# Optimization experiments

Measured on AMD Instinct MI355X. Metric: run time of the kernel, lower is better.

Reference implementation:

```python
import jax, jax.numpy as jnp
import numpy as np

D_MODEL = 1024
NUM_HEADS = 16
D_HEAD = D_MODEL // NUM_HEADS


def setup_inputs() -> dict:
    key = jax.random.key(0)
    ks = jax.random.split(key, 5)
    b, n = 4, 2048
    x = jax.random.normal(ks[0], (b, n, D_MODEL), dtype=jnp.float32)
    s = 1.0 / np.sqrt(D_MODEL)
    w_qkv = jax.random.normal(ks[1], (D_MODEL, 3 * D_MODEL), dtype=jnp.float32) * s
    b_qkv = jax.random.normal(ks[2], (3 * D_MODEL,), dtype=jnp.float32) * 0.01
    w_out = jax.random.normal(ks[3], (D_MODEL, D_MODEL), dtype=jnp.float32) * s
    b_out = jax.random.normal(ks[4], (D_MODEL,), dtype=jnp.float32) * 0.01
    return {"x": x, "w_qkv": w_qkv, "b_qkv": b_qkv, "w_out": w_out, "b_out": b_out}


def reference(x, w_qkv, b_qkv, w_out, b_out):
    b, n, _ = x.shape
    h, d = NUM_HEADS, D_HEAD
    scale = d ** -0.5
    qkv = x @ w_qkv + b_qkv                       # [b, n, 3*d_model]
    # split as (qkv, h, d) on the feature axis, matching 'b n (qkv h d)'
    qkv = qkv.reshape(b, n, 3, h, d).transpose(2, 0, 3, 1, 4)  # [3, b, h, n, d]
    q, k, v = qkv[0], qkv[1], qkv[2]
    dots = jnp.einsum('bhid,bhjd->bhij', q, k) * scale
    causal = jnp.tril(jnp.ones((n, n), dtype=bool))
    dots = jnp.where(causal[None, None], dots, -jnp.inf)
    attn = jax.nn.softmax(dots, axis=-1)
    out = jnp.einsum('bhij,bhjd->bhid', attn, v)
    out = out.transpose(0, 2, 1, 3).reshape(b, n, h * d)
    return out @ w_out + b_out
```

## Files before the change

kernel.cpp:

```cpp
#include <hip/hip_runtime.h>
#include <hip/hip_bf16.h>
#include <stdint.h>

typedef unsigned short u16;
typedef __attribute__((ext_vector_type(8))) short bf16x8;
typedef __attribute__((ext_vector_type(4))) float f32x4;
typedef __attribute__((ext_vector_type(16))) float f32x16;
typedef __attribute__((ext_vector_type(4))) short s16x4;
typedef __attribute__((ext_vector_type(2))) unsigned u32x2;

#define SEQ   2048
#define BATCH 4

#define MFMA16(a,b,c) __builtin_amdgcn_mfma_f32_16x16x32_bf16(a,b,c,0,0,0)
#define MFMA32(a,b,c) __builtin_amdgcn_mfma_f32_32x32x16_bf16(a,b,c,0,0,0)
#define EXP2F __builtin_amdgcn_exp2f

__device__ __forceinline__ u16 f2bf(float f) {
  union { float f; uint32_t u; } c{f};
  uint32_t r = c.u + 0x7fffu + ((c.u >> 16) & 1u);
  return (u16)(r >> 16);
}

__device__ __forceinline__ void gll16(const void* g, void* l) {
  __builtin_amdgcn_global_load_lds((const __attribute__((address_space(1))) void*)g,
                                   (__attribute__((address_space(3))) void*)l,
                                   16, 0, 0);
}

__device__ __forceinline__ void plswap(uint32_t &a, uint32_t &b) {
  u32x2 r = __builtin_amdgcn_permlane32_swap(a, b, false, false);
  a = r[0]; b = r[1];
}
__device__ __forceinline__ float xhalf_max(float v) {
  union { float f; uint32_t u; } c{v};
  u32x2 r = __builtin_amdgcn_permlane32_swap(c.u, c.u, false, false);
  union { uint32_t u; float f; } x{r[0]}, y{r[1]};
  return fmaxf(x.f, y.f);
}
__device__ __forceinline__ float xhalf_add(float v) {
  union { float f; uint32_t u; } c{v};
  u32x2 r = __builtin_amdgcn_permlane32_swap(c.u, c.u, false, false);
  union { uint32_t u; float f; } x{r[0]}, y{r[1]};
  return x.f + y.f;
}

__global__ __launch_bounds__(256) void k_prep(const float* __restrict__ x,
                                              u16* __restrict__ xbf,
                                              const float* __restrict__ wqkv,
                                              u16* __restrict__ wqkvT,
                                              const float* __restrict__ wout,
                                              u16* __restrict__ woutT) {
  __shared__ float tl[32][33];
  const int bid = blockIdx.x, t = threadIdx.x;
  if (bid < 4096) {
    int i = (bid * 256 + t) * 8;
    float4 a = *(const float4*)(x + i);
    float4 b = *(const float4*)(x + i + 4);
    union { u16 u[8]; bf16x8 v; } r;
    r.u[0] = f2bf(a.x); r.u[1] = f2bf(a.y); r.u[2] = f2bf(a.z); r.u[3] = f2bf(a.w);
    r.u[4] = f2bf(b.x); r.u[5] = f2bf(b.y); r.u[6] = f2bf(b.z); r.u[7] = f2bf(b.w);
    *(bf16x8*)(xbf + i) = r.v;
    return;
  }
  const float* in; u16* out; int N, idx, nx;
  if (bid < 4096 + 3072) { in = wqkv; out = wqkvT; N = 3072; idx = bid - 4096; nx = 96; }
  else                   { in = wout; out = woutT; N = 1024; idx = bid - 7168; nx = 32; }
  const int K = 1024;
  const int c0 = (idx % nx) * 32, r0 = (idx / nx) * 32;
  const int tx = t & 31, ty = t >> 5;
#pragma unroll
  for (int j = 0; j < 32; j += 8)
    tl[ty + j][tx] = in[(size_t)(r0 + ty + j) * N + c0 + tx];
  __syncthreads();
#pragma unroll
  for (int j = 0; j < 32; j += 8)
    out[(size_t)(c0 + ty + j) * K + r0 + tx] = f2bf(tl[tx][ty + j]);
}

#define SBAR  asm volatile("s_barrier" ::: "memory")
#define LGKM0 asm volatile("s_waitcnt lgkmcnt(0)" ::: "memory")
#define VM2   asm volatile("s_waitcnt vmcnt(2)" ::: "memory")
#define VM0   asm volatile("s_waitcnt vmcnt(0)" ::: "memory")
#define FEN   asm volatile("" ::: "memory")

template<int OUT_F32, int VSPLIT>
__global__ __launch_bounds__(512, 2) void k_gemm256(const u16* __restrict__ A,
                                                    const u16* __restrict__ BT,
                                                    const float* __restrict__ bias,
                                                    void* __restrict__ Cv,
                                                    u16* __restrict__ vT,
                                                    int N, int K, int NT, int TN) {
  __shared__ alignas(16) char LDS[98304];
  const int t = threadIdx.x;
  const int l = t & 63, w = t >> 6;
  const int wm = w >> 2, wn = w & 3;
  const int lr = l & 15, lg = l >> 4;

  const int nwg = gridDim.x;
  const int cpx = nwg >> 3;
  const int sb = (blockIdx.x & 7) * cpx + (blockIdx.x >> 3);
  const int brow = (sb / TN) * 256, bcol = (sb % TN) * 128;

  auto stageA = [&](int c, int h, int tt) {
#pragma unroll
    for (int i = 0; i < 2; i++) {
      int s = t + i * 512;
      int r = s >> 3, cg = s & 7;
      int grow = brow + (r >> 6) * 128 + h * 64 + (r & 63);
      int gk = tt * 64 + ((cg ^ (r & 7)) * 8);
      gll16(A + (size_t)grow * K + gk, LDS + c * 49152 + h * 16384 + s * 16);
    }
  };
  auto stageB = [&](int c, int tt) {
#pragma unroll
    for (int i = 0; i < 2; i++) {
      int s = t + i * 512;
      int r = s >> 3, cg = s & 7;
      int grow = bcol + r;
      int gk = tt * 64 + ((cg ^ (r & 7)) * 8);
      gll16(BT + (size_t)grow * K + gk, LDS + c * 49152 + 32768 + s * 16);
    }
  };

  f32x4 acc[8][2] = {};
  bf16x8 afr[4], bfr[2];

#define READ_A(c, h, ks)                                                       \
  {                                                                            \
    const char* baseA = LDS + (c) * 49152 + (h) * 16384 + (wm * 64) * 128;     \
    _Pragma("unroll") for (int mi = 0; mi < 4; mi++)                           \
      afr[mi] = *(const bf16x8*)(baseA + (mi * 16 + lr) * 128 +                \
                                 ((((ks) * 4 + lg) ^ (lr & 7)) * 16));         \
  }
#define READ_B(c, ks)                                                          \
  {                                                                            \
    const char* baseB = LDS + (c) * 49152 + 32768 + (wn * 32) * 128;           \
    _Pragma("unroll") for (int ni = 0; ni < 2; ni++)                           \
      bfr[ni] = *(const bf16x8*)(baseB + (ni * 16 + lr) * 128 +                \
                                 ((((ks) * 4 + lg) ^ (lr & 7)) * 16));         \
  }
#define DO_MFMA(H)                                                             \
  {                                                                            \
    __builtin_amdgcn_s_setprio(1);                                             \
    _Pragma("unroll") for (int mi = 0; mi < 4; mi++)                           \
      _Pragma("unroll") for (int ni = 0; ni < 2; ni++)                         \
        acc[(H)*4 + mi][ni] = MFMA16(afr[mi], bfr[ni], acc[(H)*4 + mi][ni]);   \
    __builtin_amdgcn_s_setprio(0);                                             \
  }

  stageA(0, 0, 0); FEN;
  stageB(0, 0);    FEN;
  stageA(0, 1, 0); FEN;
  VM2; SBAR;

  for (int tt = 0; tt < NT; tt++) {
    const int c = tt & 1;
    if (tt + 1 < NT) { stageA(c ^ 1, 0, tt + 1); FEN; }
    READ_A(c, 0, 0); READ_B(c, 0);
    DO_MFMA(0);
    if (tt + 1 < NT) { VM2; } else { VM0; }
    LGKM0; SBAR;
    if (tt + 1 < NT) { stageB(c ^ 1, tt + 1); FEN; }
    READ_A(c, 1, 0);
    DO_MFMA(1);
    if (tt + 1 < NT) { stageA(c ^ 1, 1, tt + 1); FEN; }
    READ_A(c, 1, 1); READ_B(c, 1);
    DO_MFMA(1);
    READ_A(c, 0, 1);
    DO_MFMA(0);
    VM2;
    LGKM0; SBAR;
  }

  const int r0 = brow + wm * 128 + lg * 4;
  const int c0 = bcol + wn * 32 + lr;
#pragma unroll
  for (int ni = 0; ni < 2; ni++) {
    const int col = c0 + ni * 16;
    float bv = bias[col];
#pragma unroll
    for (int mig = 0; mig < 8; mig++) {
      const int row = r0 + mig * 16;
      if (VSPLIT && col >= 2048) {
        const int bb = row >> 11, n0 = row & 2047;
        union { u16 u[4]; s16x4 v; } pk4;
#pragma unroll
        for (int r = 0; r < 4; r++) pk4.u[r] = f2bf(acc[mig][ni][r] + bv);
        *(s16x4*)(vT + ((size_t)(bb * 1024 + col - 2048) * SEQ + n0)) = pk4.v;
      } else {
#pragma unroll
        for (int r = 0; r < 4; r++) {
          float v = acc[mig][ni][r] + bv;
          size_t off = (size_t)(row + r) * N + col;
          if (OUT_F32) ((float*)Cv)[off] = v;
          else         ((u16*)Cv)[off]   = f2bf(v);
        }
      }
    }
  }
}
#undef READ_A
#undef READ_B
#undef DO_MFMA

__global__ __launch_bounds__(256, 2) void k_attn(const u16* __restrict__ qkv,
                                                 const u16* __restrict__ vT,
                                                 u16* __restrict__ outp) {
  __shared__ alignas(16) char SB[2][16384];
  const int t = threadIdx.x, l = t & 63, w = t >> 6;
  const int hi = l >> 5, q = l & 31;
  const int h = blockIdx.x, qp = blockIdx.y, b = blockIdx.z;
  const int bh = b * 16 + h;
  const int srow = t >> 3;
  const int csw = ((t & 7) * 16) ^ ((srow & 7) << 4);
  const int swz = (q & 7) << 4;
  const float SC = 0.18033688011112042f;

  auto STAGE = [&](char* buf, int kv0) {
    char* lK = buf + w * 1024;
    char* lV = buf + 8192 + w * 1024;
    gll16(qkv + (size_t)(b * SEQ + kv0 + srow) * 3072 + 1024 + h * 64 + (csw >> 1), lK);
    gll16(qkv + (size_t)(b * SEQ + kv0 + srow + 32) * 3072 + 1024 + h * 64 + (csw >> 1), lK + 4096);
    gll16(vT + (size_t)(bh * 64 + srow) * SEQ + kv0 + (csw >> 1), lV);
    gll16(vT + (size_t)(bh * 64 + srow + 32) * SEQ + kv0 + (csw >> 1), lV + 4096);
  };

  auto COMPUTE = [&](const char* Kb, const char* Vb, int kv0, int qr0, int qg,
                     const bf16x8* qf, f32x16& o0, f32x16& o1, f32x16& lv,
                     float& m_run) {
    f32x16 st0 = {}, st1 = {};
    __builtin_amdgcn_s_setprio(1);
#pragma unroll
    for (int c = 0; c < 4; c++) {
      const int cb = c * 32 + hi * 16;
      bf16x8 k0 = *(const bf16x8*)(Kb + q * 128 + (cb ^ swz));
      bf16x8 k1 = *(const bf16x8*)(Kb + (32 + q) * 128 + (cb ^ swz));
      st0 = MFMA32(k0, qf[c], st0);
      st1 = MFMA32(k1, qf[c], st1);
    }
    __builtin_amdgcn_s_setprio(0);
    if (kv0 + 63 > qr0) {
#pragma unroll
      for (int r = 0; r < 16; r++) {
        const int krow = (r & 3) + 8 * (r >> 2) + 4 * hi;
        if (kv0 + krow > qg)      st0[r] = -1e30f;
        if (kv0 + 32 + krow > qg) st1[r] = -1e30f;
      }
    }
    float tmx[16];
#pragma unroll
    for (int r = 0; r < 16; r++) tmx[r] = fmaxf(st0[r], st1[r]);
    float v0 = fmaxf(fmaxf(tmx[0], tmx[1]), tmx[2]);
    float v1 = fmaxf(fmaxf(tmx[3], tmx[4]), tmx[5]);
    float v2 = fmaxf(fmaxf(tmx[6], tmx[7]), tmx[8]);
    float v3 = fmaxf(fmaxf(tmx[9], tmx[10]), tmx[11]);
    float v4 = fmaxf(fmaxf(tmx[12], tmx[13]), tmx[14]);
    float v5 = fmaxf(fmaxf(v0, v1), tmx[15]);
    float v6 = fmaxf(fmaxf(v2, v3), v4);
    float v7 = fmaxf(v5, v6);
    const float vs = xhalf_max(v7) * SC;
    if (__any(vs > m_run + 8.0f)) {
      float mnew = fmaxf(m_run, vs);
      float corr = EXP2F(m_run - mnew);
      m_run = mnew;
#pragma unroll
      for (int r = 0; r < 16; r++) { o0[r] *= corr; o1[r] *= corr; lv[r] *= corr; }
    }
    f32x16 e0 = st0 * SC - m_run;
    f32x16 e1 = st1 * SC - m_run;
    f32x16 p0, p1;
#pragma unroll
    for (int r = 0; r < 16; r++) { p0[r] = EXP2F(e0[r]); p1[r] = EXP2F(e1[r]); }
    lv += p0 + p1;
#pragma unroll
    for (int khb = 0; khb < 2; khb++) {
      uint32_t pk[8];
#pragma unroll
      for (int ii = 0; ii < 8; ii++) {
        float lo = khb ? p1[2 * ii] : p0[2 * ii];
        float hf = khb ? p1[2 * ii + 1] : p0[2 * ii + 1];
        asm("v_cvt_pk_bf16_f32 %0, %1, %2" : "=v"(pk[ii]) : "v"(lo), "v"(hf));
      }
      plswap(pk[0], pk[2]); plswap(pk[1], pk[3]);
      plswap(pk[4], pk[6]); plswap(pk[5], pk[7]);
      union { uint32_t u[4]; bf16x8 v; } be, bo;
      be.u[0] = pk[0]; be.u[1] = pk[1]; be.u[2] = pk[2]; be.u[3] = pk[3];
      bo.u[0] = pk[4]; bo.u[1] = pk[5]; bo.u[2] = pk[6]; bo.u[3] = pk[7];
      __builtin_amdgcn_s_setprio(1);
#pragma unroll
      for (int kti = 0; kti < 2; kti++) {
        const int cb = (khb * 2 + kti) * 32 + hi * 16;
        bf16x8 vv0 = *(const bf16x8*)(Vb + q * 128 + (cb ^ swz));
        bf16x8 vv1 = *(const bf16x8*)(Vb + (32 + q) * 128 + (cb ^ swz));
        bf16x8 pb = kti ? bo.v : be.v;
        o0 = MFMA32(vv0, pb, o0);
        o1 = MFMA32(vv1, pb, o1);
      }
      __builtin_amdgcn_s_setprio(0);
    }
  };

  const int qtA = qp, qtB = 15 - qp;
  const int qr0A = qtA * 128 + w * 32, qgA = qr0A + q;
  const int qr0B = qtB * 128 + w * 32, qgB = qr0B + q;
  bf16x8 qfA[4], qfB[4];
#pragma unroll
  for (int c = 0; c < 4; c++) {
    qfA[c] = *(const bf16x8*)(qkv + (size_t)(b * SEQ + qgA) * 3072 + h * 64 + c * 16 + hi * 8);
    qfB[c] = *(const bf16x8*)(qkv + (size_t)(b * SEQ + qgB) * 3072 + h * 64 + c * 16 + hi * 8);
  }
  f32x16 oA0 = {}, oA1 = {}, lvA = {};
  f32x16 oB0 = {}, oB1 = {}, lvB = {};
  float mA = -1e30f, mB = -1e30f;
  const int nkvB = 2 * qtB + 2;

  STAGE(SB[0], 0);
  for (int j = 0; j < nkvB; j++) {
    const int kv0 = j * 64;
    __syncthreads();
    if (j + 1 < nkvB) STAGE(SB[(j + 1) & 1], kv0 + 64);
    const char* Kb = SB[j & 1];
    const char* Vb = Kb + 8192;
    if (kv0 <= qr0A + 31)
      COMPUTE(Kb, Vb, kv0, qr0A, qgA, qfA, oA0, oA1, lvA, mA);
    if (kv0 <= qr0B + 31)
      COMPUTE(Kb, Vb, kv0, qr0B, qgB, qfB, oB0, oB1, lvB, mB);
  }
#pragma unroll
  for (int sel = 0; sel < 2; sel++) {
    f32x16& o0 = sel ? oB0 : oA0;
    f32x16& o1 = sel ? oB1 : oA1;
    f32x16& lv = sel ? lvB : lvA;
    const int qg = sel ? qgB : qgA;
    float ls = ((lv[0] + lv[1]) + (lv[2] + lv[3])) + ((lv[4] + lv[5]) + (lv[6] + lv[7]))
             + ((lv[8] + lv[9]) + (lv[10] + lv[11])) + ((lv[12] + lv[13]) + (lv[14] + lv[15]));
    ls = xhalf_add(ls);
    const float invl = 1.0f / ls;
#pragma unroll
    for (int dh = 0; dh < 2; dh++)
#pragma unroll
      for (int jq = 0; jq < 4; jq++) {
        union { u16 u[4]; s16x4 v; } pk4;
#pragma unroll
        for (int r = 0; r < 4; r++)
          pk4.u[r] = f2bf((dh ? o1[4 * jq + r] : o0[4 * jq + r]) * invl);
        *(s16x4*)(outp + (size_t)(b * SEQ + qg) * 1024 + h * 64 + dh * 32 + jq * 8 + hi * 4) = pk4.v;
      }
  }
}

extern "C" void kernel_launch(void* const* d_in, const int* in_sizes, int n_in,
                              void* d_out, int out_size, void* d_ws, size_t ws_size,
                              hipStream_t stream) {
  const float* x     = (const float*)d_in[0];
  const float* w_qkv = (const float*)d_in[1];
  const float* b_qkv = (const float*)d_in[2];
  const float* w_out = (const float*)d_in[3];
  const float* b_out = (const float*)d_in[4];

  char* ws = (char*)d_ws;
  u16* xbf   = (u16*)(ws);
  u16* wqkvT = (u16*)(ws + (16u << 20));
  u16* woutT = (u16*)(ws + (22u << 20));
  u16* qkvb  = (u16*)(ws + (24u << 20));
  u16* vTb   = (u16*)(ws + (72u << 20));

  k_prep<<<8192, 256, 0, stream>>>(x, xbf, w_qkv, wqkvT, w_out, woutT);
  k_gemm256<0, 1><<<768, 512, 0, stream>>>(xbf, wqkvT, b_qkv, qkvb, vTb, 3072, 1024, 16, 24);
  k_attn<<<dim3(16, 8, 4), 256, 0, stream>>>(qkvb, vTb, xbf);
  k_gemm256<1, 0><<<256, 512, 0, stream>>>(xbf, woutT, b_out, d_out, nullptr, 1024, 1024, 16, 8);
}
```

Measured before the change: 160.0 us.

## Single-buffer B tile in GEMM, preload both k-slices of B into registers

The GEMM kernel drops the double-buffered B tile and keeps a single B buffer in LDS, cutting shared memory from 96 KB to 80 KB. Both k-slices of B are read into registers at the start of each iteration, before the barrier, so the next B tile can overwrite the buffer after that barrier. The aim is lower LDS use, which may let more workgroups fit per CU or ease LDS pressure. The cost is more live registers for B fragments, and the B load now has to finish within half an iteration, which may expose memory latency.

```diff
diff --git a/kernel.cpp b/kernel.cpp
--- a/kernel.cpp
+++ b/kernel.cpp
@@ -91,7 +91,7 @@
                                                     void* __restrict__ Cv,
                                                     u16* __restrict__ vT,
                                                     int N, int K, int NT, int TN) {
-  __shared__ alignas(16) char LDS[98304];
+  __shared__ alignas(16) char LDS[81920];
   const int t = threadIdx.x;
   const int l = t & 63, w = t >> 6;
   const int wm = w >> 2, wn = w & 3;
@@ -109,67 +109,68 @@
       int r = s >> 3, cg = s & 7;
       int grow = brow + (r >> 6) * 128 + h * 64 + (r & 63);
       int gk = tt * 64 + ((cg ^ (r & 7)) * 8);
-      gll16(A + (size_t)grow * K + gk, LDS + c * 49152 + h * 16384 + s * 16);
+      gll16(A + (size_t)grow * K + gk, LDS + c * 32768 + h * 16384 + s * 16);
     }
   };
-  auto stageB = [&](int c, int tt) {
+  auto stageB = [&](int tt) {
 #pragma unroll
     for (int i = 0; i < 2; i++) {
       int s = t + i * 512;
       int r = s >> 3, cg = s & 7;
       int grow = bcol + r;
       int gk = tt * 64 + ((cg ^ (r & 7)) * 8);
-      gll16(BT + (size_t)grow * K + gk, LDS + c * 49152 + 32768 + s * 16);
+      gll16(BT + (size_t)grow * K + gk, LDS + 65536 + s * 16);
     }
   };
 
   f32x4 acc[8][2] = {};
-  bf16x8 afr[4], bfr[2];
+  bf16x8 afr[4], bfr[2][2];
 
 #define READ_A(c, h, ks)                                                       \
   {                                                                            \
-    const char* baseA = LDS + (c) * 49152 + (h) * 16384 + (wm * 64) * 128;     \
+    const char* baseA = LDS + (c) * 32768 + (h) * 16384 + (wm * 64) * 128;     \
     _Pragma("unroll") for (int mi = 0; mi < 4; mi++)                           \
       afr[mi] = *(const bf16x8*)(baseA + (mi * 16 + lr) * 128 +                \
                                  ((((ks) * 4 + lg) ^ (lr & 7)) * 16));         \
   }
-#define READ_B(c, ks)                                                          \
+#define READ_B_ALL()                                                           \
   {                                                                            \
-    const char* baseB = LDS + (c) * 49152 + 32768 + (wn * 32) * 128;           \
-    _Pragma("unroll") for (int ni = 0; ni < 2; ni++)                           \
-      bfr[ni] = *(const bf16x8*)(baseB + (ni * 16 + lr) * 128 +                \
-                                 ((((ks) * 4 + lg) ^ (lr & 7)) * 16));         \
-  }
-#define DO_MFMA(H)                                                             \
+    const char* baseB = LDS + 65536 + (wn * 32) * 128;                         \
+    _Pragma("unroll") for (int ks = 0; ks < 2; ks++)                           \
+      _Pragma("unroll") for (int ni = 0; ni < 2; ni++)                         \
+        bfr[ks][ni] = *(const bf16x8*)(baseB + (ni * 16 + lr) * 128 +          \
+                                       (((ks * 4 + lg) ^ (lr & 7)) * 16));     \
+  }
+#define DO_MFMA(H, KS)                                                         \
   {                                                                            \
     __builtin_amdgcn_s_setprio(1);                                             \
     _Pragma("unroll") for (int mi = 0; mi < 4; mi++)                           \
       _Pragma("unroll") for (int ni = 0; ni < 2; ni++)                         \
-        acc[(H)*4 + mi][ni] = MFMA16(afr[mi], bfr[ni], acc[(H)*4 + mi][ni]);   \
+        acc[(H)*4 + mi][ni] = MFMA16(afr[mi], bfr[KS][ni], acc[(H)*4 + mi][ni]); \
     __builtin_amdgcn_s_setprio(0);                                             \
   }
 
   stageA(0, 0, 0); FEN;
-  stageB(0, 0);    FEN;
+  stageB(0);       FEN;
   stageA(0, 1, 0); FEN;
   VM2; SBAR;
 
   for (int tt = 0; tt < NT; tt++) {
     const int c = tt & 1;
     if (tt + 1 < NT) { stageA(c ^ 1, 0, tt + 1); FEN; }
-    READ_A(c, 0, 0); READ_B(c, 0);
-    DO_MFMA(0);
+    READ_A(c, 0, 0); READ_B_ALL();
+    DO_MFMA(0, 0);
     if (tt + 1 < NT) { VM2; } else { VM0; }
     LGKM0; SBAR;
-    if (tt + 1 < NT) { stageB(c ^ 1, tt + 1); FEN; }
+    if (tt + 1 < NT) { stageB(tt + 1); FEN; }
     READ_A(c, 1, 0);
-    DO_MFMA(1);
+    DO_MFMA(1, 0);
     if (tt + 1 < NT) { stageA(c ^ 1, 1, tt + 1); FEN; }
-    READ_A(c, 1, 1); READ_B(c, 1);
-    DO_MFMA(1);
+    READ_A(c, 1, 1);
+    DO_MFMA(1, 1);
     READ_A(c, 0, 1);
-    DO_MFMA(0);
-    VM2;
+    DO_MFMA(0, 1);
+    if (tt + 1 < NT) { VM2; } else { VM0; }
     LGKM0; SBAR;
   }
 
@@ -201,7 +202,7 @@
   }
 }
 #undef READ_A
-#undef READ_B
+#undef READ_B_ALL
 #undef DO_MFMA
 
 __global__ __launch_bounds__(256, 2) void k_attn(const u16* __restrict__ qkv,
```

Result: no change. 157.6 us (-1.5%).
